# Kernel optimization log

Measured on AMD Instinct MI355X. Metric: run time of the kernel, lower is better.

## Reference

```python
import jax, jax.numpy as jnp
import numpy as np

H = 10          # hidden_size
TAIL = 1440     # slice out[:, -1440:-1, :]


def _cell(x, h, c, w_ih, w_hh, b):
    # PyTorch LSTM gate order: i, f, g, o
    gates = x @ w_ih.T + h @ w_hh.T + b          # [B, 4H]
    i, f, g, o = jnp.split(gates, 4, axis=-1)
    c = jax.nn.sigmoid(f) * c + jax.nn.sigmoid(i) * jnp.tanh(g)
    h = jax.nn.sigmoid(o) * jnp.tanh(c)
    return h, c


def setup_inputs() -> dict:
    key = jax.random.key(0)
    ks = jax.random.split(key, 13)
    s = 1.0 / np.sqrt(H)  # PyTorch default init range

    def u(k, shape):
        return jax.random.uniform(k, shape, jnp.float32, -s, s)

    return {
        "x": jax.random.normal(ks[0], (4096, 2048), jnp.float32),
        "w_ih0": u(ks[1], (4 * H, 1)),
        "w_hh0": u(ks[2], (4 * H, H)),
        "b_ih0": u(ks[3], (4 * H,)),
        "b_hh0": u(ks[4], (4 * H,)),
        "w_ih1": u(ks[5], (4 * H, H)),
        "w_hh1": u(ks[6], (4 * H, H)),
        "b_ih1": u(ks[7], (4 * H,)),
        "b_hh1": u(ks[8], (4 * H,)),
        "fc1_w": u(ks[9], (6, H)),
        "fc1_b": u(ks[10], (6,)),
        "fc2_w": u(ks[11], (1, 6)),
        "fc2_b": u(ks[12], (1,)),
    }


def reference(x, w_ih0, w_hh0, b_ih0, b_hh0, w_ih1, w_hh1, b_ih1, b_hh1,
              fc1_w, fc1_b, fc2_w, fc2_b):
    B, T = x.shape
    xt = x[..., None].transpose(1, 0, 2)         # [T, B, 1] time-major
    b0 = b_ih0 + b_hh0
    b1 = b_ih1 + b_hh1
    z = jnp.zeros((B, H), x.dtype)

    def step(carry, xi):
        h0, c0, h1, c1 = carry
        h0, c0 = _cell(xi, h0, c0, w_ih0, w_hh0, b0)
        h1, c1 = _cell(h0, h1, c1, w_ih1, w_hh1, b1)
        return (h0, c0, h1, c1), h1

    _, ys = jax.lax.scan(step, (z, z, z, z), xt)  # ys: [T, B, H]
    out = ys.transpose(1, 0, 2)[:, T - TAIL:T - 1, :]   # [B, 1439, H]
    out = jnp.tanh(out @ fc1_w.T + fc1_b)                # [B, 1439, 6]
    out = out @ fc2_w.T + fc2_b                          # [B, 1439, 1]
    return out[..., 0]                                   # [B, 1439]
```

## Files before the change

kernel.cpp:

```cpp
#include <hip/hip_runtime.h>

typedef float v2f __attribute__((ext_vector_type(2)));

#define T_LEN 2048
#define NH    10
#define OUT_T 1439
#define TFIRST 608
#define NSEQ  4096
#define CH    8
#define NCH   (T_LEN / CH)

static __device__ __forceinline__ v2f fma2(v2f a, v2f b, v2f c) {
  return __builtin_elementwise_fma(a, b, c);
}
static __device__ __forceinline__ v2f splat2(float v) { v2f r; r.x = v; r.y = v; return r; }
static __device__ __forceinline__ v2f mulsp(v2f a, float s) { v2f r; r.x = a.x*s; r.y = a.y*s; return r; }

static __device__ __forceinline__ float fast_sigmoid(float z) {
  float e = __builtin_amdgcn_exp2f(z * -1.4426950408889634f);
  return __builtin_amdgcn_rcpf(1.0f + e);
}
static __device__ __forceinline__ float fast_tanh(float z) {
  float e = __builtin_amdgcn_exp2f(z * -2.8853900817779268f);
  return __builtin_amdgcn_rcpf(1.0f + e) * 2.0f - 1.0f;
}

#define SWZB(v, j) __uint_as_float(__builtin_amdgcn_ds_swizzle( \
    (int)__float_as_uint(v), (((j) << 5) | 0x10)))

#define ROR_F(v, N) __uint_as_float(__builtin_amdgcn_update_dpp( \
    0, (int)__float_as_uint(v), 0x120 + (N), 0xF, 0xF, true))

__global__ void __launch_bounds__(128, 2)
lstm_fused(const float* __restrict__ x,
           const float* __restrict__ w_ih0, const float* __restrict__ w_hh0,
           const float* __restrict__ b_ih0, const float* __restrict__ b_hh0,
           const float* __restrict__ w_ih1, const float* __restrict__ w_hh1,
           const float* __restrict__ b_ih1, const float* __restrict__ b_hh1,
           const float* __restrict__ fc1_w, const float* __restrict__ fc1_b,
           const float* __restrict__ fc2_w, const float* __restrict__ fc2_b,
           float* __restrict__ out)
{
  __shared__ float h0buf[2][CH][64];

  const int tid  = threadIdx.x;
  const int wid  = tid >> 6;
  const int lane = tid & 63;
  const int grp  = lane >> 4;
  const int u    = lane & 15;
  const int seq  = (int)blockIdx.x * 4 + grp;

  v2f wA_if[NH], wA_go[NH], wB_if[NH], wB_go[NH];
  v2f wx_if, wx_go, bb_if, bb_go;
  wx_if = wx_go = bb_if = bb_go = splat2(0.f);
#pragma unroll
  for (int j = 0; j < NH; ++j) {
    wA_if[j] = splat2(0.f); wA_go[j] = splat2(0.f);
    wB_if[j] = splat2(0.f); wB_go[j] = splat2(0.f);
  }

  if (u < NH) {
    const int ri = 0*NH+u, rf = 1*NH+u, rg = 2*NH+u, ro = 3*NH+u;
    if (wid == 0) {
      wx_if.x = w_ih0[ri]; wx_if.y = w_ih0[rf];
      wx_go.x = w_ih0[rg]; wx_go.y = w_ih0[ro];
      bb_if.x = b_ih0[ri] + b_hh0[ri]; bb_if.y = b_ih0[rf] + b_hh0[rf];
      bb_go.x = b_ih0[rg] + b_hh0[rg]; bb_go.y = b_ih0[ro] + b_hh0[ro];
#pragma unroll
      for (int j = 0; j < NH; ++j) {
        wA_if[j].x = w_hh0[ri*NH+j]; wA_if[j].y = w_hh0[rf*NH+j];
        wA_go[j].x = w_hh0[rg*NH+j]; wA_go[j].y = w_hh0[ro*NH+j];
      }
    } else {
      bb_if.x = b_ih1[ri] + b_hh1[ri]; bb_if.y = b_ih1[rf] + b_hh1[rf];
      bb_go.x = b_ih1[rg] + b_hh1[rg]; bb_go.y = b_ih1[ro] + b_hh1[ro];
#pragma unroll
      for (int j = 0; j < NH; ++j) {
        wA_if[j].x = w_ih1[ri*NH+j]; wA_if[j].y = w_ih1[rf*NH+j];
        wA_go[j].x = w_ih1[rg*NH+j]; wA_go[j].y = w_ih1[ro*NH+j];
        wB_if[j].x = w_hh1[ri*NH+j]; wB_if[j].y = w_hh1[rf*NH+j];
        wB_go[j].x = w_hh1[rg*NH+j]; wB_go[j].y = w_hh1[ro*NH+j];
      }
    }
  } else if (wid == 1) {
    bb_go.x = fc1_b[u - NH];
#pragma unroll
    for (int j = 0; j < NH; ++j) wB_go[j].x = fc1_w[(u - NH)*NH + j];
  }

  const float fc2wl = (wid == 1 && u >= NH) ? fc2_w[u - NH] : 0.f;
  const float fc2bl = fc2_b[0];

  const float* xp   = x + (size_t)seq * T_LEN;
  float*       outp = out + (size_t)seq * OUT_T;

  float c = 0.f;
  float r0=0.f,r1=0.f,r2=0.f,r3=0.f,r4=0.f,r5=0.f,r6=0.f,r7=0.f,r8=0.f,r9=0.f;
  float xv = (wid == 0) ? xp[0] : 0.f;

  auto a_chunk = [&](int m) {
    const int t0 = m * CH;
#pragma unroll 1
    for (int s = 0; s < CH; ++s) {
      const int t  = t0 + s;
      const int tn = (t + 1 < T_LEN) ? (t + 1) : (T_LEN - 1);
      const float xn = xp[tn];
      v2f aA = fma2(wx_if, splat2(xv), bb_if);
      v2f gA = fma2(wx_go, splat2(xv), bb_go);
      v2f aB = mulsp(wA_if[1], r1);
      v2f gB = mulsp(wA_go[1], r1);
#define L0T(j, hv, AC, GC) { const v2f sp = splat2(hv); \
      AC = fma2(wA_if[j], sp, AC); GC = fma2(wA_go[j], sp, GC); }
      L0T(0,r0,aA,gA) L0T(2,r2,aA,gA) L0T(3,r3,aB,gB) L0T(4,r4,aA,gA)
      L0T(5,r5,aB,gB) L0T(6,r6,aA,gA) L0T(7,r7,aB,gB) L0T(8,r8,aA,gA)
      L0T(9,r9,aB,gB)
#undef L0T
      const v2f gif = aA + aB;
      const v2f ggo = gA + gB;
      const float si = fast_sigmoid(gif.x);
      const float sf = fast_sigmoid(gif.y);
      const float tg = fast_tanh(ggo.x);
      const float so = fast_sigmoid(ggo.y);
      c = sf * c + si * tg;
      const float h0n = so * fast_tanh(c);
      h0buf[m & 1][s][lane] = h0n;
      r0 = SWZB(h0n,0); r1 = SWZB(h0n,1); r2 = SWZB(h0n,2); r3 = SWZB(h0n,3);
      r4 = SWZB(h0n,4); r5 = SWZB(h0n,5); r6 = SWZB(h0n,6); r7 = SWZB(h0n,7);
      r8 = SWZB(h0n,8); r9 = SWZB(h0n,9);
      xv = xn;
    }
  };

  auto b_chunk = [&](int m) {
    const int t0 = m * CH;
#pragma unroll 1
    for (int s = 0; s < CH; ++s) {
      const int t = t0 + s;
      const float* hb = &h0buf[m & 1][s][grp * 16];
      const float p0 = hb[0], p1 = hb[1], p2 = hb[2], p3 = hb[3], p4 = hb[4],
                  p5 = hb[5], p6 = hb[6], p7 = hb[7], p8 = hb[8], p9 = hb[9];
      v2f cC = fma2(wB_if[0], splat2(r0), bb_if);
      v2f hC = fma2(wB_go[0], splat2(r0), bb_go);
      v2f cD = mulsp(wB_if[1], r1);
      v2f hD = mulsp(wB_go[1], r1);
#define L1R(j, hv, AC, GC) { const v2f sp = splat2(hv); \
      AC = fma2(wB_if[j], sp, AC); GC = fma2(wB_go[j], sp, GC); }
      L1R(2,r2,cC,hC) L1R(3,r3,cD,hD) L1R(4,r4,cC,hC) L1R(5,r5,cD,hD)
      L1R(6,r6,cC,hC) L1R(7,r7,cD,hD) L1R(8,r8,cC,hC) L1R(9,r9,cD,hD)
#undef L1R
      v2f cA = mulsp(wA_if[0], p0);
      v2f hA = mulsp(wA_go[0], p0);
      v2f cB = mulsp(wA_if[1], p1);
      v2f hB = mulsp(wA_go[1], p1);
#define L1I(j, hv, AC, GC) { const v2f sp = splat2(hv); \
      AC = fma2(wA_if[j], sp, AC); GC = fma2(wA_go[j], sp, GC); }
      L1I(2,p2,cA,hA) L1I(3,p3,cB,hB) L1I(4,p4,cA,hA) L1I(5,p5,cB,hB)
      L1I(6,p6,cA,hA) L1I(7,p7,cB,hB) L1I(8,p8,cA,hA) L1I(9,p9,cB,hB)
#undef L1I
      const v2f gif = (cA + cB) + (cC + cD);
      const v2f ggo = (hA + hB) + (hC + hD);
      const float si1 = fast_sigmoid(gif.x);
      const float sf1 = fast_sigmoid(gif.y);
      const float tg1 = fast_tanh(ggo.x);
      const float so1 = fast_sigmoid(ggo.y);
      c = sf1 * c + si1 * tg1;
      const float h1n = so1 * fast_tanh(c);
      r0 = SWZB(h1n,0); r1 = SWZB(h1n,1); r2 = SWZB(h1n,2); r3 = SWZB(h1n,3);
      r4 = SWZB(h1n,4); r5 = SWZB(h1n,5); r6 = SWZB(h1n,6); r7 = SWZB(h1n,7);
      r8 = SWZB(h1n,8); r9 = SWZB(h1n,9);
      if (t > TFIRST) {
        float y = tg1 * fc2wl;
        y += ROR_F(y, 8);
        y += ROR_F(y, 4);
        y += ROR_F(y, 2);
        y += ROR_F(y, 1);
        if (u == 0) outp[t - 1 - TFIRST] = y + fc2bl;
      }
    }
  };

  if (wid == 0) a_chunk(0);
#pragma unroll 1
  for (int i = 0; i < NCH; ++i) {
    __syncthreads();
    if (wid == 0) {
      if (i + 1 < NCH) a_chunk(i + 1);
    } else {
      b_chunk(i);
    }
  }
}

extern "C" void kernel_launch(void* const* d_in, const int* in_sizes, int n_in,
                              void* d_out, int out_size, void* d_ws, size_t ws_size,
                              hipStream_t stream) {
  const float* x     = (const float*)d_in[0];
  const float* w_ih0 = (const float*)d_in[1];
  const float* w_hh0 = (const float*)d_in[2];
  const float* b_ih0 = (const float*)d_in[3];
  const float* b_hh0 = (const float*)d_in[4];
  const float* w_ih1 = (const float*)d_in[5];
  const float* w_hh1 = (const float*)d_in[6];
  const float* b_ih1 = (const float*)d_in[7];
  const float* b_hh1 = (const float*)d_in[8];
  const float* fc1_w = (const float*)d_in[9];
  const float* fc1_b = (const float*)d_in[10];
  const float* fc2_w = (const float*)d_in[11];
  const float* fc2_b = (const float*)d_in[12];
  float* out = (float*)d_out;

  lstm_fused<<<dim3(NSEQ / 4), dim3(128), 0, stream>>>(
      x, w_ih0, w_hh0, b_ih0, b_hh0, w_ih1, w_hh1, b_ih1, b_hh1,
      fc1_w, fc1_b, fc2_w, fc2_b, out);
}
```

Before: 760.2 us.

## Add third wavefront for FC head and broadcast hidden state through LDS

Moves the FC1/tanh/FC2 head off the layer-1 wavefront onto a new third wavefront, giving a three-stage pipeline (layer0, layer1, head) across chunks with one barrier per round. The head is computed from h1 stored in a new LDS double buffer. The old code's fused head had fc1 rows folded into idle lanes and applied fc2 to their tanh output; the new code computes it explicitly. The ds_swizzle broadcasts of h are replaced by an LDS store followed by vectorized float4/float2 reads, and the per-chunk step loops are fully unrolled with x read directly. This adds a wave per block and more LDS traffic in the serial recurrence path. It also risks lower occupancy under the new 192-thread launch bounds.

New measurement: 735.7 us. 1.03x faster.

```diff
diff --git a/kernel.cpp b/kernel.cpp
--- a/kernel.cpp
+++ b/kernel.cpp
@@ -9,6 +9,7 @@
 #define NSEQ  4096
 #define CH    8
 #define NCH   (T_LEN / CH)
+#define MFIRST (TFIRST / CH)
 
 static __device__ __forceinline__ v2f fma2(v2f a, v2f b, v2f c) {
   return __builtin_elementwise_fma(a, b, c);
@@ -25,13 +26,10 @@
   return __builtin_amdgcn_rcpf(1.0f + e) * 2.0f - 1.0f;
 }
 
-#define SWZB(v, j) __uint_as_float(__builtin_amdgcn_ds_swizzle( \
-    (int)__float_as_uint(v), (((j) << 5) | 0x10)))
-
 #define ROR_F(v, N) __uint_as_float(__builtin_amdgcn_update_dpp( \
     0, (int)__float_as_uint(v), 0x120 + (N), 0xF, 0xF, true))
 
-__global__ void __launch_bounds__(128, 2)
+__global__ void __launch_bounds__(192, 3)
 lstm_fused(const float* __restrict__ x,
            const float* __restrict__ w_ih0, const float* __restrict__ w_hh0,
            const float* __restrict__ b_ih0, const float* __restrict__ b_hh0,
@@ -41,76 +39,83 @@
            const float* __restrict__ fc2_w, const float* __restrict__ fc2_b,
            float* __restrict__ out)
 {
-  __shared__ float h0buf[2][CH][64];
+  __shared__ __align__(16) float h0buf[2][CH][64];
+  __shared__ __align__(16) float h1buf[2][CH][64];
 
   const int tid  = threadIdx.x;
-  const int wid  = tid >> 6;
+  const int wid  = tid / 64;
   const int lane = tid & 63;
   const int grp  = lane >> 4;
   const int u    = lane & 15;
   const int seq  = (int)blockIdx.x * 4 + grp;
 
-  v2f wA_if[NH], wA_go[NH], wB_if[NH], wB_go[NH];
+  v2f wIF[NH], wGO[NH], vIF[NH], vGO[NH];
   v2f wx_if, wx_go, bb_if, bb_go;
   wx_if = wx_go = bb_if = bb_go = splat2(0.f);
 #pragma unroll
   for (int j = 0; j < NH; ++j) {
-    wA_if[j] = splat2(0.f); wA_go[j] = splat2(0.f);
-    wB_if[j] = splat2(0.f); wB_go[j] = splat2(0.f);
+    wIF[j] = splat2(0.f); wGO[j] = splat2(0.f);
+    vIF[j] = splat2(0.f); vGO[j] = splat2(0.f);
   }
-
-  if (u < NH) {
-    const int ri = 0*NH+u, rf = 1*NH+u, rg = 2*NH+u, ro = 3*NH+u;
-    if (wid == 0) {
+  float fcw[NH];
+#pragma unroll
+  for (int j = 0; j < NH; ++j) fcw[j] = 0.f;
+  float fcb = 0.f, fc2wl = 0.f;
+  const float fc2bl = fc2_b[0];
+
+  if (wid == 0) {
+    if (u < NH) {
+      const int ri = 0*NH+u, rf = 1*NH+u, rg = 2*NH+u, ro = 3*NH+u;
       wx_if.x = w_ih0[ri]; wx_if.y = w_ih0[rf];
       wx_go.x = w_ih0[rg]; wx_go.y = w_ih0[ro];
       bb_if.x = b_ih0[ri] + b_hh0[ri]; bb_if.y = b_ih0[rf] + b_hh0[rf];
       bb_go.x = b_ih0[rg] + b_hh0[rg]; bb_go.y = b_ih0[ro] + b_hh0[ro];
 #pragma unroll
       for (int j = 0; j < NH; ++j) {
-        wA_if[j].x = w_hh0[ri*NH+j]; wA_if[j].y = w_hh0[rf*NH+j];
-        wA_go[j].x = w_hh0[rg*NH+j]; wA_go[j].y = w_hh0[ro*NH+j];
+        wIF[j].x = w_hh0[ri*NH+j]; wIF[j].y = w_hh0[rf*NH+j];
+        wGO[j].x = w_hh0[rg*NH+j]; wGO[j].y = w_hh0[ro*NH+j];
       }
-    } else {
+    }
+  } else if (wid == 1) {
+    if (u < NH) {
+      const int ri = 0*NH+u, rf = 1*NH+u, rg = 2*NH+u, ro = 3*NH+u;
       bb_if.x = b_ih1[ri] + b_hh1[ri]; bb_if.y = b_ih1[rf] + b_hh1[rf];
       bb_go.x = b_ih1[rg] + b_hh1[rg]; bb_go.y = b_ih1[ro] + b_hh1[ro];
 #pragma unroll
       for (int j = 0; j < NH; ++j) {
-        wA_if[j].x = w_ih1[ri*NH+j]; wA_if[j].y = w_ih1[rf*NH+j];
-        wA_go[j].x = w_ih1[rg*NH+j]; wA_go[j].y = w_ih1[ro*NH+j];
-        wB_if[j].x = w_hh1[ri*NH+j]; wB_if[j].y = w_hh1[rf*NH+j];
-        wB_go[j].x = w_hh1[rg*NH+j]; wB_go[j].y = w_hh1[ro*NH+j];
+        wIF[j].x = w_ih1[ri*NH+j]; wIF[j].y = w_ih1[rf*NH+j];
+        wGO[j].x = w_ih1[rg*NH+j]; wGO[j].y = w_ih1[ro*NH+j];
+        vIF[j].x = w_hh1[ri*NH+j]; vIF[j].y = w_hh1[rf*NH+j];
+        vGO[j].x = w_hh1[rg*NH+j]; vGO[j].y = w_hh1[ro*NH+j];
       }
     }
-  } else if (wid == 1) {
-    bb_go.x = fc1_b[u - NH];
-#pragma unroll
-    for (int j = 0; j < NH; ++j) wB_go[j].x = fc1_w[(u - NH)*NH + j];
+  } else {
+    if (u < 6) {
+      fcb = fc1_b[u]; fc2wl = fc2_w[u];
+#pragma unroll
+      for (int j = 0; j < NH; ++j) fcw[j] = fc1_w[u*NH + j];
+    }
   }
-
-  const float fc2wl = (wid == 1 && u >= NH) ? fc2_w[u - NH] : 0.f;
-  const float fc2bl = fc2_b[0];
 
   const float* xp   = x + (size_t)seq * T_LEN;
   float*       outp = out + (size_t)seq * OUT_T;
 
   float c = 0.f;
   float r0=0.f,r1=0.f,r2=0.f,r3=0.f,r4=0.f,r5=0.f,r6=0.f,r7=0.f,r8=0.f,r9=0.f;
-  float xv = (wid == 0) ? xp[0] : 0.f;
 
   auto a_chunk = [&](int m) {
-    const int t0 = m * CH;
-#pragma unroll 1
+    float* hb = &h0buf[m & 1][0][0];
+    const float* hr = &h0buf[m & 1][0][grp * 16];
+    const float* xq = xp + m * CH;
+#pragma unroll
     for (int s = 0; s < CH; ++s) {
-      const int t  = t0 + s;
-      const int tn = (t + 1 < T_LEN) ? (t + 1) : (T_LEN - 1);
-      const float xn = xp[tn];
+      const float xv = xq[s];
       v2f aA = fma2(wx_if, splat2(xv), bb_if);
       v2f gA = fma2(wx_go, splat2(xv), bb_go);
-      v2f aB = mulsp(wA_if[1], r1);
-      v2f gB = mulsp(wA_go[1], r1);
+      v2f aB = mulsp(wIF[1], r1);
+      v2f gB = mulsp(wGO[1], r1);
 #define L0T(j, hv, AC, GC) { const v2f sp = splat2(hv); \
-      AC = fma2(wA_if[j], sp, AC); GC = fma2(wA_go[j], sp, GC); }
+      AC = fma2(wIF[j], sp, AC); GC = fma2(wGO[j], sp, GC); }
       L0T(0,r0,aA,gA) L0T(2,r2,aA,gA) L0T(3,r3,aB,gB) L0T(4,r4,aA,gA)
       L0T(5,r5,aB,gB) L0T(6,r6,aA,gA) L0T(7,r7,aB,gB) L0T(8,r8,aA,gA)
       L0T(9,r9,aB,gB)
@@ -123,40 +128,43 @@
       const float so = fast_sigmoid(ggo.y);
       c = sf * c + si * tg;
       const float h0n = so * fast_tanh(c);
-      h0buf[m & 1][s][lane] = h0n;
-      r0 = SWZB(h0n,0); r1 = SWZB(h0n,1); r2 = SWZB(h0n,2); r3 = SWZB(h0n,3);
-      r4 = SWZB(h0n,4); r5 = SWZB(h0n,5); r6 = SWZB(h0n,6); r7 = SWZB(h0n,7);
-      r8 = SWZB(h0n,8); r9 = SWZB(h0n,9);
-      xv = xn;
+      hb[s*64 + lane] = h0n;
+      const float4 va = *(const float4*)(hr + s*64);
+      const float4 vb = *(const float4*)(hr + s*64 + 4);
+      const float2 vc = *(const float2*)(hr + s*64 + 8);
+      r0=va.x; r1=va.y; r2=va.z; r3=va.w;
+      r4=vb.x; r5=vb.y; r6=vb.z; r7=vb.w;
+      r8=vc.x; r9=vc.y;
     }
   };
 
   auto b_chunk = [&](int m) {
-    const int t0 = m * CH;
-#pragma unroll 1
+    const float* hbi = &h0buf[m & 1][0][grp * 16];
+    float* ob = &h1buf[m & 1][0][0];
+    const float* orr = &h1buf[m & 1][0][grp * 16];
+#pragma unroll
     for (int s = 0; s < CH; ++s) {
-      const int t = t0 + s;
-      const float* hb = &h0buf[m & 1][s][grp * 16];
-      const float p0 = hb[0], p1 = hb[1], p2 = hb[2], p3 = hb[3], p4 = hb[4],
-                  p5 = hb[5], p6 = hb[6], p7 = hb[7], p8 = hb[8], p9 = hb[9];
-      v2f cC = fma2(wB_if[0], splat2(r0), bb_if);
-      v2f hC = fma2(wB_go[0], splat2(r0), bb_go);
-      v2f cD = mulsp(wB_if[1], r1);
-      v2f hD = mulsp(wB_go[1], r1);
+      const float4 pa = *(const float4*)(hbi + s*64);
+      const float4 pb = *(const float4*)(hbi + s*64 + 4);
+      const float2 pc = *(const float2*)(hbi + s*64 + 8);
+      v2f cA = fma2(wIF[0], splat2(pa.x), bb_if);
+      v2f hA = fma2(wGO[0], splat2(pa.x), bb_go);
+      v2f cB = mulsp(wIF[1], pa.y);
+      v2f hB = mulsp(wGO[1], pa.y);
+#define L1I(j, hv, AC, GC) { const v2f sp = splat2(hv); \
+      AC = fma2(wIF[j], sp, AC); GC = fma2(wGO[j], sp, GC); }
+      L1I(2,pa.z,cA,hA) L1I(3,pa.w,cB,hB) L1I(4,pb.x,cA,hA) L1I(5,pb.y,cB,hB)
+      L1I(6,pb.z,cA,hA) L1I(7,pb.w,cB,hB) L1I(8,pc.x,cA,hA) L1I(9,pc.y,cB,hB)
+#undef L1I
+      v2f cC = mulsp(vIF[0], r0);
+      v2f hC = mulsp(vGO[0], r0);
+      v2f cD = mulsp(vIF[1], r1);
+      v2f hD = mulsp(vGO[1], r1);
 #define L1R(j, hv, AC, GC) { const v2f sp = splat2(hv); \
-      AC = fma2(wB_if[j], sp, AC); GC = fma2(wB_go[j], sp, GC); }
+      AC = fma2(vIF[j], sp, AC); GC = fma2(vGO[j], sp, GC); }
       L1R(2,r2,cC,hC) L1R(3,r3,cD,hD) L1R(4,r4,cC,hC) L1R(5,r5,cD,hD)
       L1R(6,r6,cC,hC) L1R(7,r7,cD,hD) L1R(8,r8,cC,hC) L1R(9,r9,cD,hD)
 #undef L1R
-      v2f cA = mulsp(wA_if[0], p0);
-      v2f hA = mulsp(wA_go[0], p0);
-      v2f cB = mulsp(wA_if[1], p1);
-      v2f hB = mulsp(wA_go[1], p1);
-#define L1I(j, hv, AC, GC) { const v2f sp = splat2(hv); \
-      AC = fma2(wA_if[j], sp, AC); GC = fma2(wA_go[j], sp, GC); }
-      L1I(2,p2,cA,hA) L1I(3,p3,cB,hB) L1I(4,p4,cA,hA) L1I(5,p5,cB,hB)
-      L1I(6,p6,cA,hA) L1I(7,p7,cB,hB) L1I(8,p8,cA,hA) L1I(9,p9,cB,hB)
-#undef L1I
       const v2f gif = (cA + cB) + (cC + cD);
       const v2f ggo = (hA + hB) + (hC + hD);
       const float si1 = fast_sigmoid(gif.x);
@@ -165,29 +173,57 @@
       const float so1 = fast_sigmoid(ggo.y);
       c = sf1 * c + si1 * tg1;
       const float h1n = so1 * fast_tanh(c);
-      r0 = SWZB(h1n,0); r1 = SWZB(h1n,1); r2 = SWZB(h1n,2); r3 = SWZB(h1n,3);
-      r4 = SWZB(h1n,4); r5 = SWZB(h1n,5); r6 = SWZB(h1n,6); r7 = SWZB(h1n,7);
-      r8 = SWZB(h1n,8); r9 = SWZB(h1n,9);
-      if (t > TFIRST) {
-        float y = tg1 * fc2wl;
+      ob[s*64 + lane] = h1n;
+      const float4 va = *(const float4*)(orr + s*64);
+      const float4 vb = *(const float4*)(orr + s*64 + 4);
+      const float2 vc = *(const float2*)(orr + s*64 + 8);
+      r0=va.x; r1=va.y; r2=va.z; r3=va.w;
+      r4=vb.x; r5=vb.y; r6=vb.z; r7=vb.w;
+      r8=vc.x; r9=vc.y;
+    }
+  };
+
+  auto c_chunk = [&](int m) {
+    const float* hb = &h1buf[m & 1][0][grp * 16];
+    const int t0 = m * CH;
+    float* oq = outp + (t0 - TFIRST);
+#pragma unroll
+    for (int s = 0; s < CH; ++s) {
+      if (t0 + s < TFIRST + OUT_T) {
+        const float4 pa = *(const float4*)(hb + s*64);
+        const float4 pb = *(const float4*)(hb + s*64 + 4);
+        const float2 pc = *(const float2*)(hb + s*64 + 8);
+        float acc = __builtin_fmaf(pa.x, fcw[0], fcb);
+        acc = __builtin_fmaf(pa.y, fcw[1], acc);
+        acc = __builtin_fmaf(pa.z, fcw[2], acc);
+        acc = __builtin_fmaf(pa.w, fcw[3], acc);
+        acc = __builtin_fmaf(pb.x, fcw[4], acc);
+        acc = __builtin_fmaf(pb.y, fcw[5], acc);
+        acc = __builtin_fmaf(pb.z, fcw[6], acc);
+        acc = __builtin_fmaf(pb.w, fcw[7], acc);
+        acc = __builtin_fmaf(pc.x, fcw[8], acc);
+        acc = __builtin_fmaf(pc.y, fcw[9], acc);
+        float y = fast_tanh(acc) * fc2wl;
         y += ROR_F(y, 8);
         y += ROR_F(y, 4);
         y += ROR_F(y, 2);
         y += ROR_F(y, 1);
-        if (u == 0) outp[t - 1 - TFIRST] = y + fc2bl;
+        if (u == 0) oq[s] = y + fc2bl;
       }
     }
   };
 
-  if (wid == 0) a_chunk(0);
 #pragma unroll 1
-  for (int i = 0; i < NCH; ++i) {
+  for (int r = 0; r < NCH + 2; ++r) {
+    if (wid == 0) {
+      if (r < NCH) a_chunk(r);
+    } else if (wid == 1) {
+      if (r >= 1 && r < NCH + 1) b_chunk(r - 1);
+    } else {
+      const int m = r - 2;
+      if (m >= MFIRST && m < NCH) c_chunk(m);
+    }
     __syncthreads();
-    if (wid == 0) {
-      if (i + 1 < NCH) a_chunk(i + 1);
-    } else {
-      b_chunk(i);
-    }
   }
 }
 
@@ -209,7 +245,7 @@
   const float* fc2_b = (const float*)d_in[12];
   float* out = (float*)d_out;
 
-  lstm_fused<<<dim3(NSEQ / 4), dim3(128), 0, stream>>>(
+  lstm_fused<<<dim3(NSEQ / 4), dim3(192), 0, stream>>>(
       x, w_ih0, w_hh0, b_ih0, b_hh0, w_ih1, w_hh1, b_ih1, b_hh1,
       fc1_w, fc1_b, fc2_w, fc2_b, out);
 }
```
